# Performance work log

Measured on AMD Instinct MI355X. Metric: run time of the kernel, lower is better.

## Reference

```python
import jax, jax.numpy as jnp
import numpy as np

NUM_EXPERTS = 8
TOP_K = 2
HIDDEN = 2048
N_TOKENS = 8192


def setup_inputs() -> dict:
    key = jax.random.key(0)
    ks = jax.random.split(key, 5)
    s = 1.0 / np.sqrt(HIDDEN)
    x = jax.random.normal(ks[0], (N_TOKENS, HIDDEN), dtype=jnp.float32)
    Wg = jax.random.normal(ks[1], (HIDDEN, NUM_EXPERTS), dtype=jnp.float32) * s
    bg = jnp.zeros((NUM_EXPERTS,), dtype=jnp.float32)
    We = jax.random.normal(ks[2], (NUM_EXPERTS, HIDDEN, HIDDEN), dtype=jnp.float32) * s
    be = jax.random.normal(ks[3], (NUM_EXPERTS, HIDDEN), dtype=jnp.float32) * 0.01
    return {"x": x, "Wg": Wg, "bg": bg, "We": We, "be": be}


def reference(x, Wg, bg, We, be):
    # Gating: softmax over experts, top-k, renormalize selected gates.
    gates = jax.nn.softmax(x @ Wg + bg, axis=-1)            # [N, E]
    topk_g, topk_i = jax.lax.top_k(gates, TOP_K)            # [N, K]
    topk_g = topk_g / jnp.sum(topk_g, axis=-1, keepdims=True)
    # Per-expert combine weight: gate value if expert selected, else 0.
    onehot = jax.nn.one_hot(topk_i, NUM_EXPERTS, dtype=x.dtype)  # [N, K, E]
    w = jnp.einsum('nk,nke->ne', topk_g, onehot)            # [N, E]
    # Dispatch/combine: weighted sum of per-expert Linear+ReLU outputs.
    out = jnp.zeros_like(x)
    for e in range(NUM_EXPERTS):  # small fixed expert count
        h = jax.nn.relu(x @ We[e] + be[e])                  # [N, D]
        out = out + w[:, e:e + 1] * h
    return out
```

## Files before the change

kernel.cpp:

```cpp
#include <hip/hip_runtime.h>
#include <hip/hip_bf16.h>

#define NT 8192
#define HD 2048
#define NE 8

typedef unsigned short u16;
typedef u16   u16x8 __attribute__((ext_vector_type(8)));
typedef short s16x8 __attribute__((ext_vector_type(8)));
typedef float f32x4 __attribute__((ext_vector_type(4)));

__device__ __forceinline__ u16 f2bf(float f) {
    unsigned u = __float_as_uint(f);
    u += 0x7fffu + ((u >> 16) & 1u);
    return (u16)(u >> 16);
}


__global__ __launch_bounds__(256) void zero_out_kernel(float4* __restrict__ out,
                                                       int* __restrict__ counts) {
    size_t i = (size_t)blockIdx.x * 256 + threadIdx.x;
    out[i] = make_float4(0.f, 0.f, 0.f, 0.f);
    if (blockIdx.x == 0 && threadIdx.x < NE) counts[threadIdx.x] = 0;
}

__global__ __launch_bounds__(256) void gating_kernel(
    const float* __restrict__ x, const float* __restrict__ Wg,
    const float* __restrict__ bg, int* __restrict__ counts,
    int* __restrict__ tok_e, float* __restrict__ tok_w)
{
    const int wave = threadIdx.x >> 6;
    const int lane = threadIdx.x & 63;
    const int t = (blockIdx.x << 2) + wave;
    const float* xr = x + (size_t)t * HD;

    float acc[NE];
    #pragma unroll
    for (int e = 0; e < NE; ++e) acc[e] = 0.f;

    for (int h = lane; h < HD; h += 64) {
        const float xv = xr[h];
        const float* wr = Wg + h * NE;
        #pragma unroll
        for (int e = 0; e < NE; ++e) acc[e] += xv * wr[e];
    }
    #pragma unroll
    for (int off = 32; off; off >>= 1) {
        #pragma unroll
        for (int e = 0; e < NE; ++e) acc[e] += __shfl_xor(acc[e], off);
    }

    if (lane == 0) {
        float l[NE];
        #pragma unroll
        for (int e = 0; e < NE; ++e) l[e] = acc[e] + bg[e];
        int i0 = 0, i1 = -1;
        float m0 = l[0], m1 = -__builtin_inff();
        #pragma unroll
        for (int e = 1; e < NE; ++e) {
            if (l[e] > m0)      { m1 = m0; i1 = i0; m0 = l[e]; i0 = e; }
            else if (l[e] > m1) { m1 = l[e]; i1 = e; }
        }
        const float ex = expf(m1 - m0);
        const float w0 = 1.f / (1.f + ex);
        const float w1 = ex  / (1.f + ex);
        tok_e[2 * t]     = i0;
        tok_e[2 * t + 1] = i1;
        tok_w[2 * t]     = w0;
        tok_w[2 * t + 1] = w1;
        atomicAdd(counts + i0, 1);
        atomicAdd(counts + i1, 1);
    }
}

__global__ void scan_kernel(const int* __restrict__ counts,
                            int* __restrict__ offsets, int* __restrict__ cursors) {
    if (threadIdx.x == 0) {
        int s = 0;
        for (int e = 0; e < NE; ++e) { offsets[e] = s; cursors[e] = s; s += counts[e]; }
    }
}

__global__ __launch_bounds__(256) void scatter_kernel(
    const int* __restrict__ tok_e, const float* __restrict__ tok_w,
    int* __restrict__ cursors, int* __restrict__ ids, float* __restrict__ wts)
{
    const int t = blockIdx.x * 256 + threadIdx.x;
    #pragma unroll
    for (int k = 0; k < 2; ++k) {
        const int e = tok_e[2 * t + k];
        const int p = atomicAdd(cursors + e, 1);
        ids[p] = t;
        wts[p] = tok_w[2 * t + k];
    }
}

#define BM 128
#define BN 128
#define BK 32
#define LDW 40

__global__ __launch_bounds__(256) void expert_gemm_kernel(
    const float* __restrict__ x, const float* __restrict__ We,
    const float* __restrict__ be, const int* __restrict__ offsets,
    const int* __restrict__ counts, const int* __restrict__ ids,
    const float* __restrict__ wts, float* __restrict__ out)
{
    const int e    = blockIdx.z;
    const int cnt  = counts[e];
    const int row0 = blockIdx.y * BM;
    if (row0 >= cnt) return;
    const int base = offsets[e];
    const int m    = min(BM, cnt - row0);
    const int n0   = blockIdx.x * BN;

    __shared__ u16   as[BM][LDW];
    __shared__ u16   bs[BN][LDW];
    __shared__ int   rtok[BM];
    __shared__ float rw[BM];

    const int tid = threadIdx.x;
    if (tid < BM) {
        const int r = tid < m ? tid : (m - 1);
        rtok[tid] = ids[base + row0 + r];
        rw[tid]   = tid < m ? wts[base + row0 + tid] : 0.f;
    }
    __syncthreads();

    const int arow_i = tid >> 1;
    const int akh    = tid & 1;
    const float* arow = x + (size_t)rtok[arow_i] * HD + akh * 16;

    const int bpr = tid & 63;
    const int bkg = tid >> 6;
    const float* bcol = We + (size_t)e * HD * HD + (size_t)bkg * 8 * HD + n0 + 2 * bpr;

    const int lane = tid & 63;
    const int wid  = tid >> 6;
    const int wm   = (wid & 1) * 64;
    const int wn   = (wid >> 1) * 64;
    const int fr   = lane & 15;
    const int fq   = lane >> 4;

    f32x4 acc[4][4] = {};

    for (int k0 = 0; k0 < HD; k0 += BK) {
        const float4 av0 = *(const float4*)(arow + k0);
        const float4 av1 = *(const float4*)(arow + k0 + 4);
        const float4 av2 = *(const float4*)(arow + k0 + 8);
        const float4 av3 = *(const float4*)(arow + k0 + 12);
        float2 bv[8];
        #pragma unroll
        for (int j = 0; j < 8; ++j)
            bv[j] = *(const float2*)(bcol + (size_t)(k0 + j) * HD);

        __syncthreads();

        const u16x8 aw0 = { f2bf(av0.x), f2bf(av0.y), f2bf(av0.z), f2bf(av0.w),
                            f2bf(av1.x), f2bf(av1.y), f2bf(av1.z), f2bf(av1.w) };
        const u16x8 aw1 = { f2bf(av2.x), f2bf(av2.y), f2bf(av2.z), f2bf(av2.w),
                            f2bf(av3.x), f2bf(av3.y), f2bf(av3.z), f2bf(av3.w) };
        *(u16x8*)&as[arow_i][akh * 16]     = aw0;
        *(u16x8*)&as[arow_i][akh * 16 + 8] = aw1;

        const u16x8 bw0 = { f2bf(bv[0].x), f2bf(bv[1].x), f2bf(bv[2].x), f2bf(bv[3].x),
                            f2bf(bv[4].x), f2bf(bv[5].x), f2bf(bv[6].x), f2bf(bv[7].x) };
        const u16x8 bw1 = { f2bf(bv[0].y), f2bf(bv[1].y), f2bf(bv[2].y), f2bf(bv[3].y),
                            f2bf(bv[4].y), f2bf(bv[5].y), f2bf(bv[6].y), f2bf(bv[7].y) };
        *(u16x8*)&bs[2 * bpr][bkg * 8]     = bw0;
        *(u16x8*)&bs[2 * bpr + 1][bkg * 8] = bw1;

        __syncthreads();

        s16x8 af[4], bfrag[4];
        #pragma unroll
        for (int f = 0; f < 4; ++f) {
            af[f]    = *(const s16x8*)&as[wm + f * 16 + fr][fq * 8];
            bfrag[f] = *(const s16x8*)&bs[wn + f * 16 + fr][fq * 8];
        }
        #pragma unroll
        for (int mf = 0; mf < 4; ++mf)
            #pragma unroll
            for (int nf = 0; nf < 4; ++nf)
                acc[mf][nf] = __builtin_amdgcn_mfma_f32_16x16x32_bf16(
                    af[mf], bfrag[nf], acc[mf][nf], 0, 0, 0);
    }

    #pragma unroll
    for (int nf = 0; nf < 4; ++nf) {
        const int   n    = n0 + wn + nf * 16 + fr;
        const float bias = be[e * HD + n];
        #pragma unroll
        for (int mf = 0; mf < 4; ++mf) {
            #pragma unroll
            for (int r = 0; r < 4; ++r) {
                const int row = wm + mf * 16 + fq * 4 + r;
                if (row < m) {
                    float h = acc[mf][nf][r] + bias;
                    h = fmaxf(h, 0.f) * rw[row];
                    atomicAdd(out + (size_t)rtok[row] * HD + n, h);
                }
            }
        }
    }
}

extern "C" void kernel_launch(void* const* d_in, const int* in_sizes, int n_in,
                              void* d_out, int out_size, void* d_ws, size_t ws_size,
                              hipStream_t stream) {
    const float* x  = (const float*)d_in[0];
    const float* Wg = (const float*)d_in[1];
    const float* bg = (const float*)d_in[2];
    const float* We = (const float*)d_in[3];
    const float* be = (const float*)d_in[4];
    float* out = (float*)d_out;

    char* ws = (char*)d_ws;
    int*   counts  = (int*)(ws);
    int*   offsets = (int*)(ws + 32);
    int*   cursors = (int*)(ws + 64);
    int*   tok_e   = (int*)(ws + 256);
    float* tok_w   = (float*)(ws + 256 + 64 * 1024);
    int*   ids     = (int*)(ws + 256 + 128 * 1024);
    float* wts     = (float*)(ws + 256 + 192 * 1024);

    zero_out_kernel<<<(NT * HD / 4) / 256, 256, 0, stream>>>((float4*)out, counts);
    gating_kernel<<<NT / 4, 256, 0, stream>>>(x, Wg, bg, counts, tok_e, tok_w);
    scan_kernel<<<1, 64, 0, stream>>>(counts, offsets, cursors);
    scatter_kernel<<<NT / 256, 256, 0, stream>>>(tok_e, tok_w, cursors, ids, wts);

    dim3 grid(HD / BN, NT / BM, NE);
    expert_gemm_kernel<<<grid, 256, 0, stream>>>(x, We, be, offsets, counts, ids, wts, out);
}
```

Measured before the change: 931.8 us.

## Pre-convert x and transposed expert weights to bf16 before the grouped GEMM

```diff
diff --git a/kernel.cpp b/kernel.cpp
--- a/kernel.cpp
+++ b/kernel.cpp
@@ -6,6 +6,7 @@
 #define NE 8
 
 typedef unsigned short u16;
+typedef u16   u16x4 __attribute__((ext_vector_type(4)));
 typedef u16   u16x8 __attribute__((ext_vector_type(8)));
 typedef short s16x8 __attribute__((ext_vector_type(8)));
 typedef float f32x4 __attribute__((ext_vector_type(4)));
@@ -16,12 +17,40 @@
     return (u16)(u >> 16);
 }
 
+#define WS_XB   (1u << 19)
+#define WS_WET  ((1u << 19) + (32u << 20))
+#define WS_REQ  ((size_t)(1u << 19) + (96u << 20))
 
 __global__ __launch_bounds__(256) void zero_out_kernel(float4* __restrict__ out,
                                                        int* __restrict__ counts) {
     size_t i = (size_t)blockIdx.x * 256 + threadIdx.x;
     out[i] = make_float4(0.f, 0.f, 0.f, 0.f);
     if (blockIdx.x == 0 && threadIdx.x < NE) counts[threadIdx.x] = 0;
+}
+
+__global__ __launch_bounds__(256) void convert_x_kernel(const float* __restrict__ x,
+                                                        u16* __restrict__ xb) {
+    size_t i = ((size_t)blockIdx.x * 256 + threadIdx.x) * 8;
+    const float4 a = *(const float4*)(x + i);
+    const float4 b = *(const float4*)(x + i + 4);
+    u16x8 v = { f2bf(a.x), f2bf(a.y), f2bf(a.z), f2bf(a.w),
+                f2bf(b.x), f2bf(b.y), f2bf(b.z), f2bf(b.w) };
+    *(u16x8*)(xb + i) = v;
+}
+
+__global__ __launch_bounds__(256) void convert_we_kernel(const float* __restrict__ We,
+                                                         u16* __restrict__ WeT) {
+    const int e = blockIdx.z, k0 = blockIdx.y * 32, n0 = blockIdx.x * 32;
+    __shared__ u16 tile[32][33];
+    const float* src = We + (size_t)e * HD * HD;
+    const int kl = threadIdx.x >> 5, nl = threadIdx.x & 31;
+    #pragma unroll
+    for (int i = 0; i < 4; ++i)
+        tile[kl + i * 8][nl] = f2bf(src[(size_t)(k0 + kl + i * 8) * HD + n0 + nl]);
+    __syncthreads();
+    const int nr = threadIdx.x >> 3, kc = (threadIdx.x & 7) * 4;
+    u16x4 v = { tile[kc][nr], tile[kc + 1][nr], tile[kc + 2][nr], tile[kc + 3][nr] };
+    *(u16x4*)(WeT + (size_t)e * HD * HD + (size_t)(n0 + nr) * HD + k0 + kc) = v;
 }
 
 __global__ __launch_bounds__(256) void gating_kernel(
@@ -100,7 +129,96 @@
 #define BK 32
 #define LDW 40
 
-__global__ __launch_bounds__(256) void expert_gemm_kernel(
+__global__ __launch_bounds__(256) void expert_gemm_bf16(
+    const u16* __restrict__ xb, const u16* __restrict__ WeT,
+    const float* __restrict__ be, const int* __restrict__ offsets,
+    const int* __restrict__ counts, const int* __restrict__ ids,
+    const float* __restrict__ wts, float* __restrict__ out)
+{
+    const int e    = blockIdx.z;
+    const int cnt  = counts[e];
+    const int row0 = blockIdx.y * BM;
+    if (row0 >= cnt) return;
+    const int base = offsets[e];
+    const int m    = min(BM, cnt - row0);
+    const int n0   = blockIdx.x * BN;
+
+    __shared__ u16   as_[BM][LDW];
+    __shared__ u16   bs[BN][LDW];
+    __shared__ int   rtok[BM];
+    __shared__ float rw[BM];
+
+    const int tid = threadIdx.x;
+    if (tid < BM) {
+        const int r = tid < m ? tid : (m - 1);
+        rtok[tid] = ids[base + row0 + r];
+        rw[tid]   = tid < m ? wts[base + row0 + tid] : 0.f;
+    }
+    __syncthreads();
+
+    const int hr = tid >> 1;
+    const int kh = (tid & 1) * 16;
+    const u16* arow = xb + (size_t)rtok[hr] * HD + kh;
+    const u16* brow = WeT + (size_t)e * HD * HD + (size_t)(n0 + hr) * HD + kh;
+
+    const int lane = tid & 63;
+    const int wid  = tid >> 6;
+    const int wm   = (wid & 1) * 64;
+    const int wn   = (wid >> 1) * 64;
+    const int fr   = lane & 15;
+    const int fq   = lane >> 4;
+
+    f32x4 acc[4][4] = {};
+
+    for (int k0 = 0; k0 < HD; k0 += BK) {
+        const u16x8 a0 = *(const u16x8*)(arow + k0);
+        const u16x8 a1 = *(const u16x8*)(arow + k0 + 8);
+        const u16x8 b0 = *(const u16x8*)(brow + k0);
+        const u16x8 b1 = *(const u16x8*)(brow + k0 + 8);
+
+        __syncthreads();
+
+        *(u16x8*)&as_[hr][kh]     = a0;
+        *(u16x8*)&as_[hr][kh + 8] = a1;
+        *(u16x8*)&bs[hr][kh]      = b0;
+        *(u16x8*)&bs[hr][kh + 8]  = b1;
+
+        __syncthreads();
+
+        s16x8 af[4], bfrag[4];
+        #pragma unroll
+        for (int f = 0; f < 4; ++f) {
+            af[f]    = *(const s16x8*)&as_[wm + f * 16 + fr][fq * 8];
+            bfrag[f] = *(const s16x8*)&bs[wn + f * 16 + fr][fq * 8];
+        }
+        #pragma unroll
+        for (int mf = 0; mf < 4; ++mf)
+            #pragma unroll
+            for (int nf = 0; nf < 4; ++nf)
+                acc[mf][nf] = __builtin_amdgcn_mfma_f32_16x16x32_bf16(
+                    af[mf], bfrag[nf], acc[mf][nf], 0, 0, 0);
+    }
+
+    #pragma unroll
+    for (int nf = 0; nf < 4; ++nf) {
+        const int   n    = n0 + wn + nf * 16 + fr;
+        const float bias = be[e * HD + n];
+        #pragma unroll
+        for (int mf = 0; mf < 4; ++mf) {
+            #pragma unroll
+            for (int r = 0; r < 4; ++r) {
+                const int row = wm + mf * 16 + fq * 4 + r;
+                if (row < m) {
+                    float h = acc[mf][nf][r] + bias;
+                    h = fmaxf(h, 0.f) * rw[row];
+                    atomicAdd(out + (size_t)rtok[row] * HD + n, h);
+                }
+            }
+        }
+    }
+}
+
+__global__ __launch_bounds__(256) void expert_gemm_fb(
     const float* __restrict__ x, const float* __restrict__ We,
     const float* __restrict__ be, const int* __restrict__ offsets,
     const int* __restrict__ counts, const int* __restrict__ ids,
@@ -114,7 +232,7 @@
     const int m    = min(BM, cnt - row0);
     const int n0   = blockIdx.x * BN;
 
-    __shared__ u16   as[BM][LDW];
+    __shared__ u16   as_[BM][LDW];
     __shared__ u16   bs[BN][LDW];
     __shared__ int   rtok[BM];
     __shared__ float rw[BM];
@@ -130,7 +248,6 @@
     const int arow_i = tid >> 1;
     const int akh    = tid & 1;
     const float* arow = x + (size_t)rtok[arow_i] * HD + akh * 16;
-
     const int bpr = tid & 63;
     const int bkg = tid >> 6;
     const float* bcol = We + (size_t)e * HD * HD + (size_t)bkg * 8 * HD + n0 + 2 * bpr;
@@ -160,9 +277,8 @@
                             f2bf(av1.x), f2bf(av1.y), f2bf(av1.z), f2bf(av1.w) };
         const u16x8 aw1 = { f2bf(av2.x), f2bf(av2.y), f2bf(av2.z), f2bf(av2.w),
                             f2bf(av3.x), f2bf(av3.y), f2bf(av3.z), f2bf(av3.w) };
-        *(u16x8*)&as[arow_i][akh * 16]     = aw0;
-        *(u16x8*)&as[arow_i][akh * 16 + 8] = aw1;
-
+        *(u16x8*)&as_[arow_i][akh * 16]     = aw0;
+        *(u16x8*)&as_[arow_i][akh * 16 + 8] = aw1;
         const u16x8 bw0 = { f2bf(bv[0].x), f2bf(bv[1].x), f2bf(bv[2].x), f2bf(bv[3].x),
                             f2bf(bv[4].x), f2bf(bv[5].x), f2bf(bv[6].x), f2bf(bv[7].x) };
         const u16x8 bw1 = { f2bf(bv[0].y), f2bf(bv[1].y), f2bf(bv[2].y), f2bf(bv[3].y),
@@ -175,7 +291,7 @@
         s16x8 af[4], bfrag[4];
         #pragma unroll
         for (int f = 0; f < 4; ++f) {
-            af[f]    = *(const s16x8*)&as[wm + f * 16 + fr][fq * 8];
+            af[f]    = *(const s16x8*)&as_[wm + f * 16 + fr][fq * 8];
             bfrag[f] = *(const s16x8*)&bs[wn + f * 16 + fr][fq * 8];
         }
         #pragma unroll
@@ -230,5 +346,14 @@
     scatter_kernel<<<NT / 256, 256, 0, stream>>>(tok_e, tok_w, cursors, ids, wts);
 
     dim3 grid(HD / BN, NT / BM, NE);
-    expert_gemm_kernel<<<grid, 256, 0, stream>>>(x, We, be, offsets, counts, ids, wts, out);
-}
+
+    if (ws_size >= WS_REQ) {
+        u16* xb  = (u16*)(ws + WS_XB);
+        u16* WeT = (u16*)(ws + WS_WET);
+        convert_x_kernel<<<NT * HD / 8 / 256, 256, 0, stream>>>(x, xb);
+        convert_we_kernel<<<dim3(HD / 32, HD / 32, NE), 256, 0, stream>>>(We, WeT);
+        expert_gemm_bf16<<<grid, 256, 0, stream>>>(xb, WeT, be, offsets, counts, ids, wts, out);
+    } else {
+        expert_gemm_fb<<<grid, 256, 0, stream>>>(x, We, be, offsets, counts, ids, wts, out);
+    }
+}
```

Result: faster. 877.0 us (-5.9%).
